# Performance work log

Hardware: AMD Instinct MI355X
Metric: run time of the kernel (lower is better)

Reference implementation:

```python
import jax, jax.numpy as jnp
import numpy as np

S, B = 16384, 1
E = 2048          # encoder_hidden_size * num_enc_direction
H = 1024          # decoder_hidden_size
L = 2             # num_layer_dec
C = 5             # num_classes


def setup_inputs() -> dict:
    key = jax.random.key(0)
    ks = jax.random.split(key, 16)
    s = lambda fan_in: 1.0 / np.sqrt(fan_in)
    inp = {
        "encoder_hiddens": jax.random.normal(ks[0], (S, B, E), jnp.float32),
        "hidden": jax.random.normal(ks[1], (L, B, H), jnp.float32),
        "c": jax.random.normal(ks[2], (L, B, H), jnp.float32),
        # attn_alpha: Linear(2H + E, 1)
        "attn_w": jax.random.uniform(ks[3], (1, 2 * H + E), jnp.float32, -s(2 * H + E), s(2 * H + E)),
        "attn_b": jax.random.uniform(ks[4], (1,), jnp.float32, -s(2 * H + E), s(2 * H + E)),
        # LSTM layer 0: input E -> H
        "w_ih_l0": jax.random.uniform(ks[5], (4 * H, E), jnp.float32, -s(H), s(H)),
        "w_hh_l0": jax.random.uniform(ks[6], (4 * H, H), jnp.float32, -s(H), s(H)),
        "b_ih_l0": jax.random.uniform(ks[7], (4 * H,), jnp.float32, -s(H), s(H)),
        "b_hh_l0": jax.random.uniform(ks[8], (4 * H,), jnp.float32, -s(H), s(H)),
        # LSTM layer 1: input H -> H
        "w_ih_l1": jax.random.uniform(ks[9], (4 * H, H), jnp.float32, -s(H), s(H)),
        "w_hh_l1": jax.random.uniform(ks[10], (4 * H, H), jnp.float32, -s(H), s(H)),
        "b_ih_l1": jax.random.uniform(ks[11], (4 * H,), jnp.float32, -s(H), s(H)),
        "b_hh_l1": jax.random.uniform(ks[12], (4 * H,), jnp.float32, -s(H), s(H)),
        # fc: Linear(H, C)
        "fc_w": jax.random.uniform(ks[13], (C, H), jnp.float32, -s(H), s(H)),
        "fc_b": jax.random.uniform(ks[14], (C,), jnp.float32, -s(H), s(H)),
    }
    return inp


def _lstm_cell(x, h, c, w_ih, w_hh, b_ih, b_hh):
    # PyTorch gate order: i, f, g, o
    gates = x @ w_ih.T + b_ih + h @ w_hh.T + b_hh  # [B, 4H]
    i, f, g, o = jnp.split(gates, 4, axis=-1)
    c2 = jax.nn.sigmoid(f) * c + jax.nn.sigmoid(i) * jnp.tanh(g)
    h2 = jax.nn.sigmoid(o) * jnp.tanh(c2)
    return h2, c2


def reference(encoder_hiddens, hidden, c, attn_w, attn_b,
              w_ih_l0, w_hh_l0, b_ih_l0, b_hh_l0,
              w_ih_l1, w_hh_l1, b_ih_l1, b_hh_l1,
              fc_w, fc_b):
    h0, c0 = hidden[0], c[0]  # [B, H]
    # Vectorized per-timestep attn_alpha(concat(h0, c0, enc_i)):
    # split attn_w columns over [h0 | c0 | enc] and fuse the static part.
    w_h, w_c, w_e = attn_w[:, :H], attn_w[:, H:2 * H], attn_w[:, 2 * H:]
    static = h0 @ w_h.T + c0 @ w_c.T + attn_b            # [B, 1]
    scores = jnp.einsum('sbe,oe->sbo', encoder_hiddens, w_e) + static  # [S, B, 1]
    # Original applies softmax over dim=1 of a [B=1, 1] tensor per step -> all ones.
    attn = jax.nn.softmax(scores, axis=-1)               # [S, B, 1], identically 1.0
    # bmm(enc[B,E,S], attn[B,S,1]) == weighted sum over S
    attn_applied = jnp.einsum('sbe,sb->be', encoder_hiddens, attn[..., 0])  # [B, E]

    # 2-layer LSTM, single timestep
    h1, c1 = _lstm_cell(attn_applied, hidden[0], c[0], w_ih_l0, w_hh_l0, b_ih_l0, b_hh_l0)
    h2, c2 = _lstm_cell(h1, hidden[1], c[1], w_ih_l1, w_hh_l1, b_ih_l1, b_hh_l1)

    out = h2  # [B, H] == out.view(1*B, H)
    return out @ fc_w.T + fc_b  # [B, C]
```

## Files before the change

### kernel.cpp

```cpp
#include <hip/hip_runtime.h>
#include <hip/hip_bf16.h>
#include <math.h>

#define S_LEN 16384
#define E_DIM 2048
#define H_DIM 1024
#define G_DIM 4096
#define C_DIM 5

#define CS_CHUNKS 512
#define CS_ROWS   (S_LEN / CS_CHUNKS)

#define WS_PART   0
#define WS_COLSUM (WS_PART + CS_CHUNKS * E_DIM)
#define WS_HH0    (WS_COLSUM + E_DIM)
#define WS_HH1    (WS_HH0 + G_DIM)
#define WS_G0     (WS_HH1 + G_DIM)
#define WS_G1     (WS_G0 + G_DIM)

typedef float fvec4 __attribute__((ext_vector_type(4)));

__device__ __forceinline__ float wave_sum(float v) {
#pragma unroll
  for (int off = 32; off > 0; off >>= 1) v += __shfl_down(v, off);
  return v;
}
__device__ __forceinline__ float dot4(float4 a, float4 b) {
  return a.x * b.x + a.y * b.y + a.z * b.z + a.w * b.w;
}
__device__ __forceinline__ float sigm(float x) { return 1.f / (1.f + expf(-x)); }

__global__ __launch_bounds__(256) void stream_k(
    const fvec4* __restrict__ enc, const float4* __restrict__ hidden,
    const float4* __restrict__ w_hh_l0,
    const float* __restrict__ b_ih_l0, const float* __restrict__ b_hh_l0,
    const float4* __restrict__ w_hh_l1,
    const float* __restrict__ b_ih_l1, const float* __restrict__ b_hh_l1,
    fvec4* __restrict__ part, float* __restrict__ hh0,
    float* __restrict__ hh1) {
  int b = blockIdx.x;
  if (b < 1024) {
    int e4 = (b & 1) * 256 + threadIdx.x;
    int chunk = b >> 1;
    fvec4 acc = {0.f, 0.f, 0.f, 0.f};
    size_t base = (size_t)chunk * CS_ROWS * 512 + e4;
#pragma unroll 8
    for (int r = 0; r < CS_ROWS; ++r) {
      fvec4 v = __builtin_nontemporal_load(&enc[base + (size_t)r * 512]);
      acc += v;
    }
    part[(size_t)chunk * 512 + e4] = acc;
  } else {
    int which = (b >= 2048) ? 1 : 0;
    int wave = threadIdx.x >> 6;
    int lane = threadIdx.x & 63;
    int row = ((b & 1023) << 2) + wave;
    const float4* w = (which ? w_hh_l1 : w_hh_l0) + (size_t)row * 256;
    const float4* h = hidden + (which ? 256 : 0);
    float a = 0.f;
#pragma unroll
    for (int k = lane; k < 256; k += 64) a += dot4(w[k], h[k]);
    a = wave_sum(a);
    if (lane == 0) {
      float bias = which ? (b_ih_l1[row] + b_hh_l1[row])
                         : (b_ih_l0[row] + b_hh_l0[row]);
      (which ? hh1 : hh0)[row] = a + bias;
    }
  }
}

__global__ __launch_bounds__(256) void colsum_final_k(
    const float* __restrict__ part, float* __restrict__ colsum) {
  __shared__ float red[4][64];
  int lane = threadIdx.x & 63;
  int grp = threadIdx.x >> 6;
  int col = blockIdx.x * 64 + lane;
  float acc = 0.f;
  int c0 = grp * (CS_CHUNKS / 4);
#pragma unroll 8
  for (int ch = c0; ch < c0 + CS_CHUNKS / 4; ++ch)
    acc += part[(size_t)ch * E_DIM + col];
  red[grp][lane] = acc;
  __syncthreads();
  if (threadIdx.x < 64) {
    float s = (red[0][lane] + red[1][lane]) + (red[2][lane] + red[3][lane]);
    colsum[col] = s;
  }
}

__global__ __launch_bounds__(256) void gates0_k(
    const float4* __restrict__ w_ih, const float4* __restrict__ x,
    const float* __restrict__ hh0, float* __restrict__ g0) {
  int wave = threadIdx.x >> 6;
  int lane = threadIdx.x & 63;
  int row = blockIdx.x * 4 + wave;
  const float4* wi = w_ih + (size_t)row * 512;
  float a = 0.f;
#pragma unroll
  for (int k = lane; k < 512; k += 64) a += dot4(wi[k], x[k]);
  a = wave_sum(a);
  if (lane == 0) g0[row] = a + hh0[row];
}

__global__ __launch_bounds__(256) void gates1_cell0_k(
    const float* __restrict__ g0, const float* __restrict__ c0,
    const float4* __restrict__ w_ih, const float* __restrict__ hh1,
    float* __restrict__ g1) {
  __shared__ __align__(16) float h1s[H_DIM];
#pragma unroll
  for (int k = 0; k < 4; ++k) {
    int j = threadIdx.x + 256 * k;
    float ig = g0[j], fg = g0[H_DIM + j], gg = g0[2 * H_DIM + j],
          og = g0[3 * H_DIM + j];
    float c2 = sigm(fg) * c0[j] + sigm(ig) * tanhf(gg);
    h1s[j] = sigm(og) * tanhf(c2);
  }
  __syncthreads();

  int wave = threadIdx.x >> 6;
  int lane = threadIdx.x & 63;
  int row = blockIdx.x * 4 + wave;
  const float4* h14 = (const float4*)h1s;
  const float4* wi = w_ih + (size_t)row * 256;
  float a = 0.f;
#pragma unroll
  for (int k = lane; k < 256; k += 64) a += dot4(wi[k], h14[k]);
  a = wave_sum(a);
  if (lane == 0) g1[row] = a + hh1[row];
}

__global__ __launch_bounds__(512) void fc_cell1_k(
    const float* __restrict__ g1, const float* __restrict__ c1,
    const float4* __restrict__ fc_w, const float* __restrict__ fc_b,
    float* __restrict__ out) {
  __shared__ __align__(16) float h2s[H_DIM];
#pragma unroll
  for (int k = 0; k < 2; ++k) {
    int j = threadIdx.x + 512 * k;
    float ig = g1[j], fg = g1[H_DIM + j], gg = g1[2 * H_DIM + j],
          og = g1[3 * H_DIM + j];
    float c2 = sigm(fg) * c1[j] + sigm(ig) * tanhf(gg);
    h2s[j] = sigm(og) * tanhf(c2);
  }
  __syncthreads();

  int wave = threadIdx.x >> 6;
  int lane = threadIdx.x & 63;
  if (wave < C_DIM) {
    const float4* h24 = (const float4*)h2s;
    const float4* wr = fc_w + (size_t)wave * 256;
    float acc = 0.f;
#pragma unroll
    for (int k = lane; k < 256; k += 64) acc += dot4(wr[k], h24[k]);
    acc = wave_sum(acc);
    if (lane == 0) out[wave] = acc + fc_b[wave];
  }
}

extern "C" void kernel_launch(void* const* d_in, const int* in_sizes, int n_in,
                              void* d_out, int out_size, void* d_ws, size_t ws_size,
                              hipStream_t stream) {
  const float* enc     = (const float*)d_in[0];
  const float* hidden  = (const float*)d_in[1];
  const float* c_in    = (const float*)d_in[2];
  const float* w_ih_l0 = (const float*)d_in[5];
  const float* w_hh_l0 = (const float*)d_in[6];
  const float* b_ih_l0 = (const float*)d_in[7];
  const float* b_hh_l0 = (const float*)d_in[8];
  const float* w_ih_l1 = (const float*)d_in[9];
  const float* w_hh_l1 = (const float*)d_in[10];
  const float* b_ih_l1 = (const float*)d_in[11];
  const float* b_hh_l1 = (const float*)d_in[12];
  const float* fc_w    = (const float*)d_in[13];
  const float* fc_b    = (const float*)d_in[14];

  float* ws = (float*)d_ws;
  float* part   = ws + WS_PART;
  float* colsum = ws + WS_COLSUM;
  float* hh0    = ws + WS_HH0;
  float* hh1    = ws + WS_HH1;
  float* g0     = ws + WS_G0;
  float* g1     = ws + WS_G1;
  float* out    = (float*)d_out;

  stream_k<<<3072, 256, 0, stream>>>(
      (const fvec4*)enc, (const float4*)hidden,
      (const float4*)w_hh_l0, b_ih_l0, b_hh_l0,
      (const float4*)w_hh_l1, b_ih_l1, b_hh_l1,
      (fvec4*)part, hh0, hh1);

  colsum_final_k<<<E_DIM / 64, 256, 0, stream>>>(part, colsum);

  gates0_k<<<G_DIM / 4, 256, 0, stream>>>(
      (const float4*)w_ih_l0, (const float4*)colsum, hh0, g0);

  gates1_cell0_k<<<G_DIM / 4, 256, 0, stream>>>(
      g0, c_in, (const float4*)w_ih_l1, hh1, g1);

  fc_cell1_k<<<1, 512, 0, stream>>>(
      g1, c_in + H_DIM, (const float4*)fc_w, fc_b, out);
}
```

Measured before the change: 56.70 us.

## Move hidden-weight GEMVs into colsum-final kernel, nontemporal weight loads, parallel fc

```diff
diff --git a/kernel.cpp b/kernel.cpp
--- a/kernel.cpp
+++ b/kernel.cpp
@@ -25,41 +25,60 @@
   for (int off = 32; off > 0; off >>= 1) v += __shfl_down(v, off);
   return v;
 }
-__device__ __forceinline__ float dot4(float4 a, float4 b) {
+__device__ __forceinline__ float dot4(fvec4 a, fvec4 b) {
   return a.x * b.x + a.y * b.y + a.z * b.z + a.w * b.w;
 }
+__device__ __forceinline__ fvec4 ntload(const fvec4* p) {
+  return __builtin_nontemporal_load(p);
+}
 __device__ __forceinline__ float sigm(float x) { return 1.f / (1.f + expf(-x)); }
 
-__global__ __launch_bounds__(256) void stream_k(
-    const fvec4* __restrict__ enc, const float4* __restrict__ hidden,
-    const float4* __restrict__ w_hh_l0,
+__global__ __launch_bounds__(256) void colsum_partial_k(
+    const fvec4* __restrict__ enc, fvec4* __restrict__ part) {
+  int e4 = (blockIdx.x & 1) * 256 + threadIdx.x;
+  int chunk = blockIdx.x >> 1;
+  fvec4 acc = {0.f, 0.f, 0.f, 0.f};
+  size_t base = (size_t)chunk * CS_ROWS * 512 + e4;
+#pragma unroll 16
+  for (int r = 0; r < CS_ROWS; ++r) acc += ntload(&enc[base + (size_t)r * 512]);
+  part[(size_t)chunk * 512 + e4] = acc;
+}
+
+__global__ __launch_bounds__(256) void final_hh_k(
+    const float* __restrict__ part, const fvec4* __restrict__ hidden,
+    const fvec4* __restrict__ w_hh_l0,
     const float* __restrict__ b_ih_l0, const float* __restrict__ b_hh_l0,
-    const float4* __restrict__ w_hh_l1,
+    const fvec4* __restrict__ w_hh_l1,
     const float* __restrict__ b_ih_l1, const float* __restrict__ b_hh_l1,
-    fvec4* __restrict__ part, float* __restrict__ hh0,
+    float* __restrict__ colsum, float* __restrict__ hh0,
     float* __restrict__ hh1) {
   int b = blockIdx.x;
-  if (b < 1024) {
-    int e4 = (b & 1) * 256 + threadIdx.x;
-    int chunk = b >> 1;
-    fvec4 acc = {0.f, 0.f, 0.f, 0.f};
-    size_t base = (size_t)chunk * CS_ROWS * 512 + e4;
+  if (b < 32) {
+    __shared__ float red[4][64];
+    int lane = threadIdx.x & 63;
+    int grp = threadIdx.x >> 6;
+    int col = b * 64 + lane;
+    float acc = 0.f;
+    int c0 = grp * (CS_CHUNKS / 4);
 #pragma unroll 8
-    for (int r = 0; r < CS_ROWS; ++r) {
-      fvec4 v = __builtin_nontemporal_load(&enc[base + (size_t)r * 512]);
-      acc += v;
+    for (int ch = c0; ch < c0 + CS_CHUNKS / 4; ++ch)
+      acc += part[(size_t)ch * E_DIM + col];
+    red[grp][lane] = acc;
+    __syncthreads();
+    if (threadIdx.x < 64) {
+      float s = (red[0][lane] + red[1][lane]) + (red[2][lane] + red[3][lane]);
+      colsum[col] = s;
     }
-    part[(size_t)chunk * 512 + e4] = acc;
   } else {
-    int which = (b >= 2048) ? 1 : 0;
+    int which = (b >= 32 + 1024) ? 1 : 0;
     int wave = threadIdx.x >> 6;
     int lane = threadIdx.x & 63;
-    int row = ((b & 1023) << 2) + wave;
-    const float4* w = (which ? w_hh_l1 : w_hh_l0) + (size_t)row * 256;
-    const float4* h = hidden + (which ? 256 : 0);
+    int row = ((b - 32) & 1023) * 4 + wave;
+    const fvec4* w = (which ? w_hh_l1 : w_hh_l0) + (size_t)row * 256;
+    const fvec4* h = hidden + (which ? 256 : 0);
     float a = 0.f;
 #pragma unroll
-    for (int k = lane; k < 256; k += 64) a += dot4(w[k], h[k]);
+    for (int k = lane; k < 256; k += 64) a += dot4(ntload(&w[k]), h[k]);
     a = wave_sum(a);
     if (lane == 0) {
       float bias = which ? (b_ih_l1[row] + b_hh_l1[row])
@@ -69,42 +88,23 @@
   }
 }
 
-__global__ __launch_bounds__(256) void colsum_final_k(
-    const float* __restrict__ part, float* __restrict__ colsum) {
-  __shared__ float red[4][64];
-  int lane = threadIdx.x & 63;
-  int grp = threadIdx.x >> 6;
-  int col = blockIdx.x * 64 + lane;
-  float acc = 0.f;
-  int c0 = grp * (CS_CHUNKS / 4);
-#pragma unroll 8
-  for (int ch = c0; ch < c0 + CS_CHUNKS / 4; ++ch)
-    acc += part[(size_t)ch * E_DIM + col];
-  red[grp][lane] = acc;
-  __syncthreads();
-  if (threadIdx.x < 64) {
-    float s = (red[0][lane] + red[1][lane]) + (red[2][lane] + red[3][lane]);
-    colsum[col] = s;
-  }
-}
-
 __global__ __launch_bounds__(256) void gates0_k(
-    const float4* __restrict__ w_ih, const float4* __restrict__ x,
+    const fvec4* __restrict__ w_ih, const fvec4* __restrict__ x,
     const float* __restrict__ hh0, float* __restrict__ g0) {
   int wave = threadIdx.x >> 6;
   int lane = threadIdx.x & 63;
   int row = blockIdx.x * 4 + wave;
-  const float4* wi = w_ih + (size_t)row * 512;
+  const fvec4* wi = w_ih + (size_t)row * 512;
   float a = 0.f;
 #pragma unroll
-  for (int k = lane; k < 512; k += 64) a += dot4(wi[k], x[k]);
+  for (int k = lane; k < 512; k += 64) a += dot4(ntload(&wi[k]), x[k]);
   a = wave_sum(a);
   if (lane == 0) g0[row] = a + hh0[row];
 }
 
 __global__ __launch_bounds__(256) void gates1_cell0_k(
     const float* __restrict__ g0, const float* __restrict__ c0,
-    const float4* __restrict__ w_ih, const float* __restrict__ hh1,
+    const fvec4* __restrict__ w_ih, const float* __restrict__ hh1,
     float* __restrict__ g1) {
   __shared__ __align__(16) float h1s[H_DIM];
 #pragma unroll
@@ -120,20 +120,21 @@
   int wave = threadIdx.x >> 6;
   int lane = threadIdx.x & 63;
   int row = blockIdx.x * 4 + wave;
-  const float4* h14 = (const float4*)h1s;
-  const float4* wi = w_ih + (size_t)row * 256;
+  const fvec4* h14 = (const fvec4*)h1s;
+  const fvec4* wi = w_ih + (size_t)row * 256;
   float a = 0.f;
 #pragma unroll
-  for (int k = lane; k < 256; k += 64) a += dot4(wi[k], h14[k]);
+  for (int k = lane; k < 256; k += 64) a += dot4(ntload(&wi[k]), h14[k]);
   a = wave_sum(a);
   if (lane == 0) g1[row] = a + hh1[row];
 }
 
 __global__ __launch_bounds__(512) void fc_cell1_k(
     const float* __restrict__ g1, const float* __restrict__ c1,
-    const float4* __restrict__ fc_w, const float* __restrict__ fc_b,
+    const float* __restrict__ fc_w, const float* __restrict__ fc_b,
     float* __restrict__ out) {
   __shared__ __align__(16) float h2s[H_DIM];
+  __shared__ float red[8];
 #pragma unroll
   for (int k = 0; k < 2; ++k) {
     int j = threadIdx.x + 512 * k;
@@ -144,16 +145,19 @@
   }
   __syncthreads();
 
+  int r = blockIdx.x;
   int wave = threadIdx.x >> 6;
   int lane = threadIdx.x & 63;
-  if (wave < C_DIM) {
-    const float4* h24 = (const float4*)h2s;
-    const float4* wr = fc_w + (size_t)wave * 256;
-    float acc = 0.f;
-#pragma unroll
-    for (int k = lane; k < 256; k += 64) acc += dot4(wr[k], h24[k]);
-    acc = wave_sum(acc);
-    if (lane == 0) out[wave] = acc + fc_b[wave];
+  const float* wr = fc_w + (size_t)r * H_DIM;
+  float a = wr[threadIdx.x] * h2s[threadIdx.x] +
+            wr[threadIdx.x + 512] * h2s[threadIdx.x + 512];
+  a = wave_sum(a);
+  if (lane == 0) red[wave] = a;
+  __syncthreads();
+  if (threadIdx.x == 0) {
+    float s = ((red[0] + red[1]) + (red[2] + red[3])) +
+              ((red[4] + red[5]) + (red[6] + red[7]));
+    out[r] = s + fc_b[r];
   }
 }
 
@@ -183,20 +187,21 @@
   float* g1     = ws + WS_G1;
   float* out    = (float*)d_out;
 
-  stream_k<<<3072, 256, 0, stream>>>(
-      (const fvec4*)enc, (const float4*)hidden,
-      (const float4*)w_hh_l0, b_ih_l0, b_hh_l0,
-      (const float4*)w_hh_l1, b_ih_l1, b_hh_l1,
-      (fvec4*)part, hh0, hh1);
-
-  colsum_final_k<<<E_DIM / 64, 256, 0, stream>>>(part, colsum);
+  colsum_partial_k<<<2 * CS_CHUNKS, 256, 0, stream>>>(
+      (const fvec4*)enc, (fvec4*)part);
+
+  final_hh_k<<<32 + 2 * 1024, 256, 0, stream>>>(
+      part, (const fvec4*)hidden,
+      (const fvec4*)w_hh_l0, b_ih_l0, b_hh_l0,
+      (const fvec4*)w_hh_l1, b_ih_l1, b_hh_l1,
+      colsum, hh0, hh1);
 
   gates0_k<<<G_DIM / 4, 256, 0, stream>>>(
-      (const float4*)w_ih_l0, (const float4*)colsum, hh0, g0);
+      (const fvec4*)w_ih_l0, (const fvec4*)colsum, hh0, g0);
 
   gates1_cell0_k<<<G_DIM / 4, 256, 0, stream>>>(
-      g0, c_in, (const float4*)w_ih_l1, hh1, g1);
-
-  fc_cell1_k<<<1, 512, 0, stream>>>(
-      g1, c_in + H_DIM, (const float4*)fc_w, fc_b, out);
-}
+      g0, c_in, (const fvec4*)w_ih_l1, hh1, g1);
+
+  fc_cell1_k<<<C_DIM, 512, 0, stream>>>(
+      g1, c_in + H_DIM, fc_w, fc_b, out);
+}
```

Result: faster. 55.49 us (-2.1%).
